# Kernel optimization log

Measured on AMD Instinct MI355X. Metric: run time of the kernel, lower is better.

## Reference

```python
import jax, jax.numpy as jnp
import numpy as np

N, E, D, C, L, G = 50000, 1600000, 128, 10, 4, 512
BN_EPS = 1e-5


def setup_inputs() -> dict:
    key = jax.random.key(0)
    ks = jax.random.split(key, 16)
    s = 0.05  # weight init scale
    inp = {
        "x": jax.random.normal(ks[0], (N, D), dtype=jnp.float32),
        "edge_index": jax.random.randint(ks[1], (2, E), 0, N, dtype=jnp.int32),
        "batch": jnp.sort(jax.random.randint(ks[2], (N,), 0, G, dtype=jnp.int32)),
        "num_graphs": G,
        # GINConv inner MLP params (layer 0 input dim == D since num_features == num_hidden)
        "conv_W1": jax.random.normal(ks[3], (L, D, D), dtype=jnp.float32) * s,
        "conv_b1": jnp.zeros((L, D), dtype=jnp.float32),
        "conv_bn_g": jnp.ones((L, D), dtype=jnp.float32),
        "conv_bn_b": jnp.zeros((L, D), dtype=jnp.float32),
        "conv_W2": jax.random.normal(ks[4], (L, D, D), dtype=jnp.float32) * s,
        "conv_b2": jnp.zeros((L, D), dtype=jnp.float32),
        # outer BatchNorm after each conv
        "bn_g": jnp.ones((L, D), dtype=jnp.float32),
        "bn_b": jnp.zeros((L, D), dtype=jnp.float32),
        # per-scale classifier heads (L+1 of them; fcs[0] input dim == num_features == D)
        "fc_W": jax.random.normal(ks[5], (L + 1, D, C), dtype=jnp.float32) * s,
        "fc_b": jnp.zeros((L + 1, C), dtype=jnp.float32),
    }
    return inp


def _bn(h, g, b):
    # BatchNorm1d in training mode: batch stats over nodes, biased variance
    m = h.mean(axis=0)
    v = jnp.mean((h - m) ** 2, axis=0)
    return (h - m) * jax.lax.rsqrt(v + BN_EPS) * g + b


def reference(x, edge_index, batch, num_graphs, conv_W1, conv_b1, conv_bn_g,
              conv_bn_b, conv_W2, conv_b2, bn_g, bn_b, fc_W, fc_b):
    n_nodes = x.shape[0]
    src, dst = edge_index[0], edge_index[1]
    outs = [x]
    h = x
    for i in range(L):
        # GINConv (eps=0, aggr='add'): mlp(x + scatter_add of neighbor features)
        agg = jax.ops.segment_sum(h[src], dst, num_segments=n_nodes)  # [N, D]
        z = h + agg
        z = z @ conv_W1[i] + conv_b1[i]
        z = jax.nn.relu(_bn(z, conv_bn_g[i], conv_bn_b[i]))
        z = z @ conv_W2[i] + conv_b2[i]
        h = jax.nn.relu(_bn(z, bn_g[i], bn_b[i]))
        outs.append(h)
    out = None
    for i, o in enumerate(outs):
        pooled = jax.ops.segment_sum(o, batch, num_segments=num_graphs)  # [G, D]
        logits = pooled @ fc_W[i] + fc_b[i]
        out = logits if out is None else out + logits
    return jax.nn.log_softmax(out, axis=-1)
```

## Files before the change

kernel.cpp:

```cpp
#include <hip/hip_runtime.h>

#define NN 50000
#define EE 1600000
#define DD 128
#define CC 10
#define LLAY 4
#define GG 512
#define GD (GG*DD)
#define NB 196
#define BK_EDGES 1600
#define BUCKCAP 16000
#define NSUB 16
#define SUBW 3125
#define WPAD 136

static constexpr float BN_EPS = 1e-5f;
static constexpr float INV_N = 1.0f / (float)NN;

typedef __bf16 bf16x8 __attribute__((ext_vector_type(8)));
typedef float f32x4 __attribute__((ext_vector_type(4)));

static __device__ __forceinline__ float bflo(unsigned u){ return __uint_as_float(u << 16); }
static __device__ __forceinline__ float bfhi(unsigned u){ return __uint_as_float(u & 0xffff0000u); }
static __device__ __forceinline__ unsigned short f2bf(float f){
    unsigned u = __float_as_uint(f);
    return (unsigned short)((u + 0x7fffu + ((u >> 16) & 1u)) >> 16);
}
static __device__ __forceinline__ unsigned packbf(float a, float b){
    return (unsigned)f2bf(a) | ((unsigned)f2bf(b) << 16);
}
static __device__ __forceinline__ bf16x8 ldfrag(const unsigned short* p){
    union { uint4 u; bf16x8 b; } t; t.u = *(const uint4*)p; return t.b;
}
static __device__ __forceinline__ bf16x8 asfrag(uint4 u){
    union { uint4 u; bf16x8 b; } t; t.u = u; return t.b;
}


__global__ void zero_k(int* p, int n){
    int i = blockIdx.x * 256 + threadIdx.x;
    if (i < n) p[i] = 0;
}

__global__ void wprep_k(const float* __restrict__ W1, const float* __restrict__ W2,
                        unsigned short* __restrict__ Wtall){
    int idx = blockIdx.x * 256 + threadIdx.x;
    int mat = idx >> 14; int rr = idx & 16383;
    int k = rr >> 7; int j = rr & 127;
    const float* Wsrc = (mat < 4) ? (W1 + mat * 16384) : (W2 + (mat - 4) * 16384);
    Wtall[mat * 16384 + j * 128 + k] = f2bf(Wsrc[k * 128 + j]);
}

__global__ void gsearch_k(const int* __restrict__ batch, int* __restrict__ gstart){
    int g = blockIdx.x * 256 + threadIdx.x;
    if (g <= GG){
        int lo = 0, hi = NN;
        while (lo < hi){ int mid = (lo + hi) >> 1; if (batch[mid] < g) lo = mid + 1; else hi = mid; }
        gstart[g] = lo;
    }
}

__global__ __launch_bounds__(256) void binA_k(const int* __restrict__ srcA,
                                              const int* __restrict__ dstA,
                                              int* __restrict__ bucketCur,
                                              unsigned* __restrict__ binned){
    __shared__ int cnt[NB], bas[NB], off[NB];
    int tid = threadIdx.x;
    if (tid < NB){ cnt[tid] = 0; off[tid] = 0; }
    __syncthreads();
    int e0 = blockIdx.x * BK_EDGES;
    for (int i = tid; i < BK_EDGES; i += 256){
        int e = e0 + i;
        if (e < EE) atomicAdd(&cnt[dstA[e] >> 8], 1);
    }
    __syncthreads();
    if (tid < NB && cnt[tid] > 0) bas[tid] = atomicAdd(&bucketCur[tid], cnt[tid]);
    __syncthreads();
    for (int i = tid; i < BK_EDGES; i += 256){
        int e = e0 + i;
        if (e < EE){
            int d = dstA[e]; int b = d >> 8;
            int p = b * BUCKCAP + bas[b] + atomicAdd(&off[b], 1);
            binned[p] = (unsigned)srcA[e] | ((unsigned)(d & 255) << 17);
        }
    }
}

__global__ __launch_bounds__(256) void bscan_k(const int* __restrict__ bucketCur,
                                               int* __restrict__ bucketBase,
                                               int* __restrict__ rp){
    __shared__ int lds[256];
    int t = threadIdx.x;
    int v = (t < NB) ? bucketCur[t] : 0;
    lds[t] = v; __syncthreads();
    for (int o = 1; o < 256; o <<= 1){
        int xv = 0; if (t >= o) xv = lds[t - o];
        __syncthreads(); lds[t] += xv; __syncthreads();
    }
    int excl = lds[t] - v;
    if (t < NB) bucketBase[t] = excl;
    if (t == 0){ bucketBase[NB] = EE; rp[NN] = EE; }
}

__global__ __launch_bounds__(1024) void binB_k(const unsigned* __restrict__ binned,
                                               const int* __restrict__ bucketCur,
                                               const int* __restrict__ bucketBase,
                                               int* __restrict__ rp,
                                               int* __restrict__ ssort){
    __shared__ int c16[256 * NSUB];
    __shared__ int b16[256 * NSUB];
    __shared__ int nt[256];
    int b = blockIdx.x, tid = threadIdx.x;
    int nb0 = b * 256;
    int nmax = NN - nb0; if (nmax > 256) nmax = 256;
    for (int i = tid; i < 256 * NSUB; i += 1024) c16[i] = 0;
    __syncthreads();
    int cntb = bucketCur[b];
    int src0 = b * BUCKCAP;
    int base = bucketBase[b];
    for (int i = tid; i < cntb; i += 1024){
        unsigned u = binned[src0 + i];
        int src = (int)(u & 0x1FFFFu); int dl = (int)(u >> 17);
        atomicAdd(&c16[dl * NSUB + src / SUBW], 1);
    }
    __syncthreads();
    int cc[NSUB]; int tot = 0;
    if (tid < 256){
        #pragma unroll
        for (int k = 0; k < NSUB; k++){ cc[k] = c16[tid * NSUB + k]; tot += cc[k]; }
        nt[tid] = tot;
    }
    __syncthreads();
    for (int o = 1; o < 256; o <<= 1){
        int xv = 0;
        if (tid < 256 && tid >= o) xv = nt[tid - o];
        __syncthreads();
        if (tid < 256) nt[tid] += xv;
        __syncthreads();
    }
    if (tid < 256){
        int p = base + nt[tid] - tot;
        if (tid < nmax) rp[nb0 + tid] = p;
        int run = p;
        #pragma unroll
        for (int k = 0; k < NSUB; k++){ b16[tid * NSUB + k] = run; run += cc[k]; }
    }
    __syncthreads();
    for (int i = tid; i < 256 * NSUB; i += 1024) c16[i] = 0;
    __syncthreads();
    for (int i = tid; i < cntb; i += 1024){
        unsigned u = binned[src0 + i];
        int src = (int)(u & 0x1FFFFu); int dl = (int)(u >> 17);
        int t = src / SUBW;
        int pos = b16[dl * NSUB + t] + atomicAdd(&c16[dl * NSUB + t], 1);
        ssort[pos] = src;
    }
}

__global__ __launch_bounds__(256) void convxpool_k(const float2* __restrict__ x2,
                                                   const int* __restrict__ gstart,
                                                   unsigned* __restrict__ h32,
                                                   float* __restrict__ outp){
    __shared__ float sd[512];
    int b = blockIdx.x; int gid = b >> 2, chunk = b & 3;
    int tid = threadIdx.x; int c = tid & 63, rs = tid >> 6;
    int s = gstart[gid], e = gstart[gid + 1];
    float a0 = 0.f, a1 = 0.f;
    for (int n = s + chunk * 4 + rs; n < e; n += 16){
        float2 v = x2[n * 64 + c];
        h32[n * 64 + c] = packbf(v.x, v.y);
        a0 += v.x; a1 += v.y;
    }
    sd[tid] = a0; sd[256 + tid] = a1; __syncthreads();
    if (tid < 64){
        float r0 = 0.f, r1 = 0.f;
        #pragma unroll
        for (int k2 = 0; k2 < 4; k2++){ r0 += sd[tid + 64 * k2]; r1 += sd[256 + tid + 64 * k2]; }
        atomicAdd(&outp[gid * 128 + 2 * tid], r0);
        atomicAdd(&outp[gid * 128 + 2 * tid + 1], r1);
    }
}


__global__ __launch_bounds__(256) void agg_k(const unsigned* __restrict__ h32,
                                             const int* __restrict__ rp,
                                             const int* __restrict__ ssort,
                                             unsigned* __restrict__ z32,
                                             float* __restrict__ zstats){
    int tid = threadIdx.x;
    if (blockIdx.x == 0) zstats[tid] = 0.f;
    int n = blockIdx.x * 4 + (tid >> 6);
    int lane = tid & 63;
    unsigned self = h32[n * 64 + lane];
    float ax = bflo(self), ay = bfhi(self);
    int e  = __builtin_amdgcn_readfirstlane(rp[n]);
    int e1 = __builtin_amdgcn_readfirstlane(rp[n + 1]);
    for (; e + 15 < e1; e += 16){
        int sA[16];
        #pragma unroll
        for (int k = 0; k < 16; k++) sA[k] = ssort[e + k];
        unsigned uA[16];
        #pragma unroll
        for (int k = 0; k < 16; k++) uA[k] = h32[sA[k] * 64 + lane];
        #pragma unroll
        for (int k = 0; k < 16; k++){ ax += bflo(uA[k]); ay += bfhi(uA[k]); }
    }
    for (; e + 3 < e1; e += 4){
        int s0 = ssort[e], s1 = ssort[e + 1], s2 = ssort[e + 2], s3 = ssort[e + 3];
        unsigned u0 = h32[s0 * 64 + lane];
        unsigned u1 = h32[s1 * 64 + lane];
        unsigned u2 = h32[s2 * 64 + lane];
        unsigned u3 = h32[s3 * 64 + lane];
        ax += bflo(u0) + bflo(u1); ay += bfhi(u0) + bfhi(u1);
        ax += bflo(u2) + bflo(u3); ay += bfhi(u2) + bfhi(u3);
    }
    for (; e < e1; ++e){
        unsigned u0 = h32[ssort[e] * 64 + lane];
        ax += bflo(u0); ay += bfhi(u0);
    }
    z32[n * 64 + lane] = packbf(ax, ay);
}

template<int TR>
__global__ __launch_bounds__(256) void gemm_k(const unsigned* __restrict__ A32,
                                              const unsigned short* __restrict__ Wtg,
                                              const float* __restrict__ bias,
                                              unsigned short* __restrict__ Cst,
                                              const float* __restrict__ stats,
                                              const float* __restrict__ gma,
                                              const float* __restrict__ bta,
                                              float* __restrict__ ostats,
                                              float* __restrict__ zstats,
                                              float* __restrict__ zpool){
    __shared__ __align__(16) unsigned short Wl[64 * WPAD];
    __shared__ float sred[512];
    __shared__ __align__(16) float sl[128], tl[128];
    int tid = threadIdx.x;
    int slice = blockIdx.x & 1;
    int tileb = blockIdx.x >> 1;

    int wv = tid >> 6, lane = tid & 63;
    int rowbase = tileb * 128 + wv * 32;
    int r0 = rowbase + (lane & 15);
    int r1 = r0 + 16;
    int kd = (lane >> 4) * 4;
    uint4 va[4], vb[4];
    #pragma unroll
    for (int ks = 0; ks < 4; ks++){
        va[ks] = (r0 < NN) ? *(const uint4*)(A32 + r0 * 64 + ks * 16 + kd) : make_uint4(0,0,0,0);
        vb[ks] = (r1 < NN) ? *(const uint4*)(A32 + r1 * 64 + ks * 16 + kd) : make_uint4(0,0,0,0);
    }

    if (blockIdx.x == 0 && zstats) zstats[tid] = 0.f;
    if (zpool && blockIdx.x < 256) zpool[blockIdx.x * 256 + tid] = 0.f;
    {
        const uint4* src = (const uint4*)(Wtg + slice * 64 * 128);
        uint4* dst = (uint4*)Wl;
        #pragma unroll
        for (int i = 0; i < 4; i++){
            int idx = tid + 256 * i;
            int row = idx >> 4, c16 = idx & 15;
            dst[row * (WPAD / 8) + c16] = src[idx];
        }
    }
    if (TR && tid < 128){
        float mean = stats[tid] * INV_N;
        float q    = stats[128 + tid] * INV_N;
        float inv  = rsqrtf(q - mean * mean + BN_EPS);
        float s    = gma[tid] * inv;
        sl[tid] = s; tl[tid] = bta[tid] - mean * s;
    }
    __syncthreads();

    if (TR){
        #pragma unroll
        for (int ks = 0; ks < 4; ks++){
            int q = ks * 8 + (lane >> 4) * 2;
            float4 sA = ((const float4*)sl)[q], sB = ((const float4*)sl)[q + 1];
            float4 tA = ((const float4*)tl)[q], tB = ((const float4*)tl)[q + 1];
            float fs[8] = {sA.x, sA.y, sA.z, sA.w, sB.x, sB.y, sB.z, sB.w};
            float ft[8] = {tA.x, tA.y, tA.z, tA.w, tB.x, tB.y, tB.z, tB.w};
            unsigned* pa = (unsigned*)&va[ks];
            unsigned* pb = (unsigned*)&vb[ks];
            #pragma unroll
            for (int c = 0; c < 4; c++){
                float f0 = fmaxf(bflo(pa[c]) * fs[2*c] + ft[2*c], 0.f);
                float f1 = fmaxf(bfhi(pa[c]) * fs[2*c+1] + ft[2*c+1], 0.f);
                pa[c] = packbf(f0, f1);
                f0 = fmaxf(bflo(pb[c]) * fs[2*c] + ft[2*c], 0.f);
                f1 = fmaxf(bfhi(pb[c]) * fs[2*c+1] + ft[2*c+1], 0.f);
                pb[c] = packbf(f0, f1);
            }
        }
    }

    f32x4 acc[2][4];
    #pragma unroll
    for (int a = 0; a < 2; a++)
        #pragma unroll
        for (int b = 0; b < 4; b++) acc[a][b] = (f32x4){0.f, 0.f, 0.f, 0.f};

    #pragma unroll
    for (int ks = 0; ks < 4; ks++){
        int wk = ks * 32 + (lane >> 4) * 8;
        bf16x8 a0 = asfrag(va[ks]);
        bf16x8 a1 = asfrag(vb[ks]);
        #pragma unroll
        for (int ct = 0; ct < 4; ++ct){
            bf16x8 b = ldfrag(&Wl[(ct * 16 + (lane & 15)) * WPAD + wk]);
            acc[0][ct] = __builtin_amdgcn_mfma_f32_16x16x32_bf16(a0, b, acc[0][ct], 0, 0, 0);
            acc[1][ct] = __builtin_amdgcn_mfma_f32_16x16x32_bf16(a1, b, acc[1][ct], 0, 0, 0);
        }
    }

    int cl = lane & 15, rq = lane >> 4;
    float colS[4], colQ[4];
    #pragma unroll
    for (int ct = 0; ct < 4; ++ct){
        int col = slice * 64 + ct * 16 + cl;
        float bv = bias[col];
        float ps = 0.f, pq = 0.f;
        #pragma unroll
        for (int rt = 0; rt < 2; ++rt){
            #pragma unroll
            for (int rr2 = 0; rr2 < 4; ++rr2){
                int grow = rowbase + rt * 16 + rq * 4 + rr2;
                if (grow < NN){
                    float val = acc[rt][ct][rr2] + bv;
                    Cst[grow * 128 + col] = f2bf(val);
                    ps += val; pq += val * val;
                }
            }
        }
        ps += __shfl_xor(ps, 16); pq += __shfl_xor(pq, 16);
        ps += __shfl_xor(ps, 32); pq += __shfl_xor(pq, 32);
        colS[ct] = ps; colQ[ct] = pq;
    }
    if (rq == 0){
        #pragma unroll
        for (int ct = 0; ct < 4; ++ct){
            sred[wv * 64 + ct * 16 + cl]       = colS[ct];
            sred[256 + wv * 64 + ct * 16 + cl] = colQ[ct];
        }
    }
    __syncthreads();
    if (tid < 64){
        float s1 = sred[tid] + sred[64 + tid] + sred[128 + tid] + sred[192 + tid];
        float s2 = sred[256 + tid] + sred[320 + tid] + sred[384 + tid] + sred[448 + tid];
        atomicAdd(&ostats[slice * 64 + tid], s1);
        atomicAdd(&ostats[128 + slice * 64 + tid], s2);
    }
}

__global__ __launch_bounds__(256) void ewpool_k(const unsigned* __restrict__ z32,
                                                const float* __restrict__ stats,
                                                const float* __restrict__ g,
                                                const float* __restrict__ b,
                                                const int* __restrict__ gstart,
                                                unsigned* __restrict__ h32,
                                                float* __restrict__ outp){
    __shared__ float sd[512];
    int blk = blockIdx.x; int gid = blk >> 2, chunk = blk & 3;
    int tid = threadIdx.x;
    int c = tid & 63, rs = tid >> 6;
    int c2 = c * 2;
    float m0 = stats[c2] * INV_N,     q0 = stats[128 + c2] * INV_N;
    float inv0 = rsqrtf(q0 - m0 * m0 + BN_EPS);
    float s0 = g[c2] * inv0, t0 = b[c2] - m0 * s0;
    float m1 = stats[c2 + 1] * INV_N, q1 = stats[129 + c2] * INV_N;
    float inv1 = rsqrtf(q1 - m1 * m1 + BN_EPS);
    float s1 = g[c2 + 1] * inv1, t1 = b[c2 + 1] - m1 * s1;
    int s = gstart[gid], e = gstart[gid + 1];
    float a0 = 0.f, a1 = 0.f;
    int n = s + chunk * 4 + rs;
    for (; n + 16 < e; n += 32){
        unsigned u0 = z32[n * 64 + c];
        unsigned u1 = z32[(n + 16) * 64 + c];
        float f0, f1;
        f0 = fmaxf(bflo(u0) * s0 + t0, 0.f); f1 = fmaxf(bfhi(u0) * s1 + t1, 0.f);
        h32[n * 64 + c] = packbf(f0, f1); a0 += f0; a1 += f1;
        f0 = fmaxf(bflo(u1) * s0 + t0, 0.f); f1 = fmaxf(bfhi(u1) * s1 + t1, 0.f);
        h32[(n + 16) * 64 + c] = packbf(f0, f1); a0 += f0; a1 += f1;
    }
    for (; n < e; n += 16){
        unsigned u = z32[n * 64 + c];
        float f0 = fmaxf(bflo(u) * s0 + t0, 0.f);
        float f1 = fmaxf(bfhi(u) * s1 + t1, 0.f);
        h32[n * 64 + c] = packbf(f0, f1);
        a0 += f0; a1 += f1;
    }
    sd[tid] = a0; sd[256 + tid] = a1; __syncthreads();
    if (tid < 64){
        float r0 = 0.f, r1 = 0.f;
        #pragma unroll
        for (int k2 = 0; k2 < 4; k2++){ r0 += sd[tid + 64 * k2]; r1 += sd[256 + tid + 64 * k2]; }
        atomicAdd(&outp[gid * 128 + 2 * tid], r0);
        atomicAdd(&outp[gid * 128 + 2 * tid + 1], r1);
    }
}

__global__ __launch_bounds__(64) void final_k(const float* __restrict__ pooled,
                                              const float* __restrict__ fcW,
                                              const float* __restrict__ fcb,
                                              float* __restrict__ out){
    int g = blockIdx.x, l = threadIdx.x;
    float p0[5], p1[5];
    #pragma unroll
    for (int i = 0; i < 5; i++){
        p0[i] = pooled[i * GD + g * 128 + l];
        p1[i] = pooled[i * GD + g * 128 + 64 + l];
    }
    float lg[10];
    #pragma unroll
    for (int c2 = 0; c2 < 10; c2++){
        float s = 0;
        #pragma unroll
        for (int i = 0; i < 5; i++){
            s += p0[i] * fcW[(i * 128 + l) * 10 + c2];
            s += p1[i] * fcW[(i * 128 + 64 + l) * 10 + c2];
        }
        #pragma unroll
        for (int off = 32; off >= 1; off >>= 1) s += __shfl_down(s, off);
        lg[c2] = s;
    }
    if (l == 0){
        #pragma unroll
        for (int c2 = 0; c2 < 10; c2++){
            float bs = 0;
            #pragma unroll
            for (int i = 0; i < 5; i++) bs += fcb[i * 10 + c2];
            lg[c2] += bs;
        }
        float mx = lg[0];
        #pragma unroll
        for (int c2 = 1; c2 < 10; c2++) mx = fmaxf(mx, lg[c2]);
        float se = 0;
        #pragma unroll
        for (int c2 = 0; c2 < 10; c2++) se += expf(lg[c2] - mx);
        float lse = mx + logf(se);
        #pragma unroll
        for (int c2 = 0; c2 < 10; c2++) out[g * 10 + c2] = lg[c2] - lse;
    }
}


extern "C" void kernel_launch(void* const* d_in, const int* in_sizes, int n_in,
                              void* d_out, int out_size, void* d_ws, size_t ws_size,
                              hipStream_t stream){
    (void)in_sizes; (void)n_in; (void)out_size; (void)ws_size;
    const float* x     = (const float*)d_in[0];
    const int*   ei    = (const int*)d_in[1];
    const int*   batch = (const int*)d_in[2];
    const float* cW1   = (const float*)d_in[4];
    const float* cb1   = (const float*)d_in[5];
    const float* cbng  = (const float*)d_in[6];
    const float* cbnb  = (const float*)d_in[7];
    const float* cW2   = (const float*)d_in[8];
    const float* cb2   = (const float*)d_in[9];
    const float* bng   = (const float*)d_in[10];
    const float* bnb   = (const float*)d_in[11];
    const float* fcW   = (const float*)d_in[12];
    const float* fcb   = (const float*)d_in[13];

    char* base = (char*)d_ws;
    size_t off = 0;
    auto alloc = [&](size_t bytes) -> void* {
        void* p = base + off;
        off = (off + bytes + 255) & ~(size_t)255;
        return p;
    };
    unsigned*       hB     = (unsigned*)alloc((size_t)NN * 64 * 4);
    unsigned*       zA     = (unsigned*)alloc((size_t)NN * 64 * 4);
    unsigned*       zB     = (unsigned*)alloc((size_t)NN * 64 * 4);
    unsigned short* Wtall  = (unsigned short*)alloc(8 * 16384 * 2);
    int*            ssort  = (int*)alloc((size_t)EE * 4);
    int*            rp     = (int*)alloc((NN + 1) * 4);
    int*            gstart = (int*)alloc((GG + 1) * 4);
    int*            bucketBase = (int*)alloc((NB + 1) * 4);
    int*            bucketCur  = (int*)alloc(NB * 4);
    float*          pooled = (float*)alloc((size_t)5 * GD * 4);
    float*          stats1 = (float*)alloc(256 * 4);
    float*          stats2 = (float*)alloc(256 * 4);
    unsigned*       binned = (unsigned*)zB;

    int zwords = (int)(((char*)(pooled + GD) - (char*)bucketCur) / 4);

    zero_k<<<(zwords + 255) / 256, 256, 0, stream>>>(bucketCur, zwords);
    wprep_k<<<512, 256, 0, stream>>>(cW1, cW2, Wtall);
    gsearch_k<<<3, 256, 0, stream>>>(batch, gstart);
    binA_k<<<(EE + BK_EDGES - 1) / BK_EDGES, 256, 0, stream>>>(ei, ei + EE, bucketCur, binned);
    bscan_k<<<1, 256, 0, stream>>>(bucketCur, bucketBase, rp);
    binB_k<<<NB, 1024, 0, stream>>>(binned, bucketCur, bucketBase, rp, ssort);
    convxpool_k<<<4 * GG, 256, 0, stream>>>((const float2*)x, gstart, hB, pooled);

    const int gemmGrid = 2 * ((NN + 127) / 128);
    for (int i = 0; i < LLAY; i++){
        agg_k<<<NN / 4, 256, 0, stream>>>(hB, rp, ssort, zA, stats1);
        gemm_k<0><<<gemmGrid, 256, 0, stream>>>(zA, Wtall + i * 16384, cb1 + i * 128,
                                                (unsigned short*)zB,
                                                nullptr, nullptr, nullptr, stats1, stats2, nullptr);
        gemm_k<1><<<gemmGrid, 256, 0, stream>>>(zB, Wtall + (4 + i) * 16384, cb2 + i * 128,
                                                (unsigned short*)zA,
                                                stats1, cbng + i * 128, cbnb + i * 128, stats2, nullptr,
                                                pooled + (size_t)(i + 1) * GD);
        ewpool_k<<<4 * GG, 256, 0, stream>>>(zA, stats2, bng + i * 128, bnb + i * 128,
                                             gstart, hB, pooled + (size_t)(i + 1) * GD);
    }
    final_k<<<GG, 64, 0, stream>>>(pooled, fcW, fcb, (float*)d_out);
}
```

Before: 544.7 us.

## Vectorize neighbor gather with 16-byte loads and add XCD-aware block swizzle

The aggregation kernel now has each 64-lane wavefront split into four groups of 16 lanes. Each lane loads a uint4, so one wavefront gathers four neighbor rows per instruction instead of one. The per-group partial sums are combined with cross-lane shuffles, and one group adds the node's own features and writes the result. Block indices are also remapped so that consecutive nodes land on the same XCD, which should improve L2 locality. The change cuts load instruction count and raises bytes in flight, at the cost of shuffle reductions and idle lanes in the tail and in the final write.

After: 557.4 us. +2.3%, slower.

```diff
diff --git a/kernel.cpp b/kernel.cpp
--- a/kernel.cpp
+++ b/kernel.cpp
@@ -189,36 +189,67 @@
                                              float* __restrict__ zstats){
     int tid = threadIdx.x;
     if (blockIdx.x == 0) zstats[tid] = 0.f;
-    int n = blockIdx.x * 4 + (tid >> 6);
+    const int q = (NN / 4) >> 3, r = (NN / 4) & 7;
+    int xcd = blockIdx.x & 7, ord = blockIdx.x >> 3;
+    int swz = (xcd < r) ? (xcd * (q + 1) + ord)
+                        : (r * (q + 1) + (xcd - r) * q + ord);
+    int n = swz * 4 + (tid >> 6);
     int lane = tid & 63;
-    unsigned self = h32[n * 64 + lane];
-    float ax = bflo(self), ay = bfhi(self);
+    int grp = lane >> 4;
+    int cq  = lane & 15;
+    const uint4* hv = (const uint4*)h32;
     int e  = __builtin_amdgcn_readfirstlane(rp[n]);
     int e1 = __builtin_amdgcn_readfirstlane(rp[n + 1]);
+    float ac[8];
+    #pragma unroll
+    for (int i = 0; i < 8; i++) ac[i] = 0.f;
     for (; e + 15 < e1; e += 16){
-        int sA[16];
-        #pragma unroll
-        for (int k = 0; k < 16; k++) sA[k] = ssort[e + k];
-        unsigned uA[16];
-        #pragma unroll
-        for (int k = 0; k < 16; k++) uA[k] = h32[sA[k] * 64 + lane];
-        #pragma unroll
-        for (int k = 0; k < 16; k++){ ax += bflo(uA[k]); ay += bfhi(uA[k]); }
+        int s[4]; uint4 v[4];
+        #pragma unroll
+        for (int k = 0; k < 4; k++) s[k] = ssort[e + k * 4 + grp];
+        #pragma unroll
+        for (int k = 0; k < 4; k++) v[k] = hv[s[k] * 16 + cq];
+        #pragma unroll
+        for (int k = 0; k < 4; k++){
+            ac[0] += bflo(v[k].x); ac[1] += bfhi(v[k].x);
+            ac[2] += bflo(v[k].y); ac[3] += bfhi(v[k].y);
+            ac[4] += bflo(v[k].z); ac[5] += bfhi(v[k].z);
+            ac[6] += bflo(v[k].w); ac[7] += bfhi(v[k].w);
+        }
     }
     for (; e + 3 < e1; e += 4){
-        int s0 = ssort[e], s1 = ssort[e + 1], s2 = ssort[e + 2], s3 = ssort[e + 3];
-        unsigned u0 = h32[s0 * 64 + lane];
-        unsigned u1 = h32[s1 * 64 + lane];
-        unsigned u2 = h32[s2 * 64 + lane];
-        unsigned u3 = h32[s3 * 64 + lane];
-        ax += bflo(u0) + bflo(u1); ay += bfhi(u0) + bfhi(u1);
-        ax += bflo(u2) + bflo(u3); ay += bfhi(u2) + bfhi(u3);
-    }
-    for (; e < e1; ++e){
-        unsigned u0 = h32[ssort[e] * 64 + lane];
-        ax += bflo(u0); ay += bfhi(u0);
-    }
-    z32[n * 64 + lane] = packbf(ax, ay);
+        int s0 = ssort[e + grp];
+        uint4 v0 = hv[s0 * 16 + cq];
+        ac[0] += bflo(v0.x); ac[1] += bfhi(v0.x);
+        ac[2] += bflo(v0.y); ac[3] += bfhi(v0.y);
+        ac[4] += bflo(v0.z); ac[5] += bfhi(v0.z);
+        ac[6] += bflo(v0.w); ac[7] += bfhi(v0.w);
+    }
+    {
+        int rem = e1 - e;
+        if (grp < rem){
+            int s0 = ssort[e + grp];
+            uint4 v0 = hv[s0 * 16 + cq];
+            ac[0] += bflo(v0.x); ac[1] += bfhi(v0.x);
+            ac[2] += bflo(v0.y); ac[3] += bfhi(v0.y);
+            ac[4] += bflo(v0.z); ac[5] += bfhi(v0.z);
+            ac[6] += bflo(v0.w); ac[7] += bfhi(v0.w);
+        }
+    }
+    #pragma unroll
+    for (int i = 0; i < 8; i++){
+        ac[i] += __shfl_xor(ac[i], 16);
+        ac[i] += __shfl_xor(ac[i], 32);
+    }
+    if (grp == 0){
+        uint4 sv = hv[n * 16 + cq];
+        uint4 o;
+        o.x = packbf(ac[0] + bflo(sv.x), ac[1] + bfhi(sv.x));
+        o.y = packbf(ac[2] + bflo(sv.y), ac[3] + bfhi(sv.y));
+        o.z = packbf(ac[4] + bflo(sv.z), ac[5] + bfhi(sv.z));
+        o.w = packbf(ac[6] + bflo(sv.w), ac[7] + bfhi(sv.w));
+        ((uint4*)z32)[n * 16 + cq] = o;
+    }
 }
 
 template<int TR>
```

## Split neighbor aggregation across XCDs by feature quarter with 16-bit edge indices

Applied to the files above, without the earlier changes.

Aggregation now maps block IDs to XCDs so that each pair of XCDs gathers only one quarter of the feature columns for half the nodes. This keeps each XCD's gather working set small enough to fit in its L2. Each wave processes 16 edges at once with 16-byte vector loads and reduces the partial sums with cross-lane shuffles. The sorted source indices are stored as 16-bit values, which halves index traffic. The cost is four times as many blocks, repeated index reads per feature quarter, and shuffle reduction overhead.

Result: slower. 692.5 us (+27.1%).

```diff
diff --git a/kernel.cpp b/kernel.cpp
--- a/kernel.cpp
+++ b/kernel.cpp
@@ -106,7 +106,7 @@
                                                const int* __restrict__ bucketCur,
                                                const int* __restrict__ bucketBase,
                                                int* __restrict__ rp,
-                                               int* __restrict__ ssort){
+                                               unsigned short* __restrict__ ssort16){
     __shared__ int c16[256 * NSUB];
     __shared__ int b16[256 * NSUB];
     __shared__ int nt[256];
@@ -153,7 +153,7 @@
         int src = (int)(u & 0x1FFFFu); int dl = (int)(u >> 17);
         int t = src / SUBW;
         int pos = b16[dl * NSUB + t] + atomicAdd(&c16[dl * NSUB + t], 1);
-        ssort[pos] = src;
+        ssort16[pos] = (unsigned short)src;
     }
 }
 
@@ -184,41 +184,72 @@
 
 __global__ __launch_bounds__(256) void agg_k(const unsigned* __restrict__ h32,
                                              const int* __restrict__ rp,
-                                             const int* __restrict__ ssort,
+                                             const unsigned short* __restrict__ ssort16,
                                              unsigned* __restrict__ z32,
                                              float* __restrict__ zstats){
     int tid = threadIdx.x;
     if (blockIdx.x == 0) zstats[tid] = 0.f;
-    int n = blockIdx.x * 4 + (tid >> 6);
+    int xcd = blockIdx.x & 7, ord = blockIdx.x >> 3;
+    int g = xcd >> 1, d = xcd & 1;
+    int n = d * (NN / 2) + ord * 4 + (tid >> 6);
     int lane = tid & 63;
-    unsigned self = h32[n * 64 + lane];
-    float ax = bflo(self), ay = bfhi(self);
+    int eslot = lane >> 2;
+    int c = lane & 3;
+    int sbase = g * 4 + c;
+    const uint4* hv = (const uint4*)h32;
     int e  = __builtin_amdgcn_readfirstlane(rp[n]);
     int e1 = __builtin_amdgcn_readfirstlane(rp[n + 1]);
-    for (; e + 15 < e1; e += 16){
-        int sA[16];
-        #pragma unroll
-        for (int k = 0; k < 16; k++) sA[k] = ssort[e + k];
-        unsigned uA[16];
-        #pragma unroll
-        for (int k = 0; k < 16; k++) uA[k] = h32[sA[k] * 64 + lane];
-        #pragma unroll
-        for (int k = 0; k < 16; k++){ ax += bflo(uA[k]); ay += bfhi(uA[k]); }
-    }
-    for (; e + 3 < e1; e += 4){
-        int s0 = ssort[e], s1 = ssort[e + 1], s2 = ssort[e + 2], s3 = ssort[e + 3];
-        unsigned u0 = h32[s0 * 64 + lane];
-        unsigned u1 = h32[s1 * 64 + lane];
-        unsigned u2 = h32[s2 * 64 + lane];
-        unsigned u3 = h32[s3 * 64 + lane];
-        ax += bflo(u0) + bflo(u1); ay += bfhi(u0) + bfhi(u1);
-        ax += bflo(u2) + bflo(u3); ay += bfhi(u2) + bfhi(u3);
-    }
-    for (; e < e1; ++e){
-        unsigned u0 = h32[ssort[e] * 64 + lane];
-        ax += bflo(u0); ay += bfhi(u0);
-    }
-    z32[n * 64 + lane] = packbf(ax, ay);
+    float ac[8];
+    #pragma unroll
+    for (int i = 0; i < 8; i++) ac[i] = 0.f;
+    for (; e + 31 < e1; e += 32){
+        int sA = (int)ssort16[e + eslot];
+        int sB = (int)ssort16[e + 16 + eslot];
+        uint4 vA = hv[sA * 16 + sbase];
+        uint4 vB = hv[sB * 16 + sbase];
+        ac[0] += bflo(vA.x); ac[1] += bfhi(vA.x);
+        ac[2] += bflo(vA.y); ac[3] += bfhi(vA.y);
+        ac[4] += bflo(vA.z); ac[5] += bfhi(vA.z);
+        ac[6] += bflo(vA.w); ac[7] += bfhi(vA.w);
+        ac[0] += bflo(vB.x); ac[1] += bfhi(vB.x);
+        ac[2] += bflo(vB.y); ac[3] += bfhi(vB.y);
+        ac[4] += bflo(vB.z); ac[5] += bfhi(vB.z);
+        ac[6] += bflo(vB.w); ac[7] += bfhi(vB.w);
+    }
+    if (e + 15 < e1){
+        int sA = (int)ssort16[e + eslot];
+        uint4 vA = hv[sA * 16 + sbase];
+        ac[0] += bflo(vA.x); ac[1] += bfhi(vA.x);
+        ac[2] += bflo(vA.y); ac[3] += bfhi(vA.y);
+        ac[4] += bflo(vA.z); ac[5] += bfhi(vA.z);
+        ac[6] += bflo(vA.w); ac[7] += bfhi(vA.w);
+        e += 16;
+    }
+    int rem = e1 - e;
+    if (eslot < rem){
+        int sA = (int)ssort16[e + eslot];
+        uint4 vA = hv[sA * 16 + sbase];
+        ac[0] += bflo(vA.x); ac[1] += bfhi(vA.x);
+        ac[2] += bflo(vA.y); ac[3] += bfhi(vA.y);
+        ac[4] += bflo(vA.z); ac[5] += bfhi(vA.z);
+        ac[6] += bflo(vA.w); ac[7] += bfhi(vA.w);
+    }
+    #pragma unroll
+    for (int i = 0; i < 8; i++){
+        ac[i] += __shfl_xor(ac[i], 4);
+        ac[i] += __shfl_xor(ac[i], 8);
+        ac[i] += __shfl_xor(ac[i], 16);
+        ac[i] += __shfl_xor(ac[i], 32);
+    }
+    if (lane < 4){
+        uint4 sv = hv[n * 16 + sbase];
+        uint4 o;
+        o.x = packbf(ac[0] + bflo(sv.x), ac[1] + bfhi(sv.x));
+        o.y = packbf(ac[2] + bflo(sv.y), ac[3] + bfhi(sv.y));
+        o.z = packbf(ac[4] + bflo(sv.z), ac[5] + bfhi(sv.z));
+        o.w = packbf(ac[6] + bflo(sv.w), ac[7] + bfhi(sv.w));
+        ((uint4*)z32)[n * 16 + sbase] = o;
+    }
 }
 
 template<int TR>
@@ -473,7 +504,7 @@
     unsigned*       zA     = (unsigned*)alloc((size_t)NN * 64 * 4);
     unsigned*       zB     = (unsigned*)alloc((size_t)NN * 64 * 4);
     unsigned short* Wtall  = (unsigned short*)alloc(8 * 16384 * 2);
-    int*            ssort  = (int*)alloc((size_t)EE * 4);
+    unsigned short* ssort16 = (unsigned short*)alloc((size_t)EE * 2);
     int*            rp     = (int*)alloc((NN + 1) * 4);
     int*            gstart = (int*)alloc((GG + 1) * 4);
     int*            bucketBase = (int*)alloc((NB + 1) * 4);
@@ -490,12 +521,12 @@
     gsearch_k<<<3, 256, 0, stream>>>(batch, gstart);
     binA_k<<<(EE + BK_EDGES - 1) / BK_EDGES, 256, 0, stream>>>(ei, ei + EE, bucketCur, binned);
     bscan_k<<<1, 256, 0, stream>>>(bucketCur, bucketBase, rp);
-    binB_k<<<NB, 1024, 0, stream>>>(binned, bucketCur, bucketBase, rp, ssort);
+    binB_k<<<NB, 1024, 0, stream>>>(binned, bucketCur, bucketBase, rp, ssort16);
     convxpool_k<<<4 * GG, 256, 0, stream>>>((const float2*)x, gstart, hB, pooled);
 
     const int gemmGrid = 2 * ((NN + 127) / 128);
     for (int i = 0; i < LLAY; i++){
-        agg_k<<<NN / 4, 256, 0, stream>>>(hB, rp, ssort, zA, stats1);
+        agg_k<<<NN, 256, 0, stream>>>(hB, rp, ssort16, zA, stats1);
         gemm_k<0><<<gemmGrid, 256, 0, stream>>>(zA, Wtall + i * 16384, cb1 + i * 128,
                                                 (unsigned short*)zB,
                                                 nullptr, nullptr, nullptr, stats1, stats2, nullptr);
```

## Fuse neighbor aggregation with first GEMM and pre-zero per-layer stats buffers

Applied to the files above, without the earlier changes.

Merges the gather-sum aggregation kernel and the first MLP GEMM into a single kernel. Each 512-thread block aggregates 128 nodes into shared memory, then runs bf16 MFMA against both weight halves and writes the output plus BN statistics, so the aggregated tensor never makes a round trip through global memory and one launch per layer is removed. The stats buffers become per-layer and are zeroed once up front instead of inside kernels. In exchange, each block's GEMM phase waits on its slowest node's gather, and the larger shared-memory footprint may reduce occupancy.

Measured after the change: 564.6 us. 1.04x slower.

```diff
diff --git a/kernel.cpp b/kernel.cpp
--- a/kernel.cpp
+++ b/kernel.cpp
@@ -13,6 +13,7 @@
 #define NSUB 16
 #define SUBW 3125
 #define WPAD 136
+#define ZPAD 68
 
 static constexpr float BN_EPS = 1e-5f;
 static constexpr float INV_N = 1.0f / (float)NN;
@@ -182,43 +183,140 @@
 }
 
 
-__global__ __launch_bounds__(256) void agg_k(const unsigned* __restrict__ h32,
-                                             const int* __restrict__ rp,
-                                             const int* __restrict__ ssort,
-                                             unsigned* __restrict__ z32,
-                                             float* __restrict__ zstats){
+__global__ __launch_bounds__(512, 6) void aggemm_k(const unsigned* __restrict__ h32,
+                                                   const int* __restrict__ rp,
+                                                   const int* __restrict__ ssort,
+                                                   const unsigned short* __restrict__ Wtg,
+                                                   const float* __restrict__ bias,
+                                                   unsigned short* __restrict__ Cst,
+                                                   float* __restrict__ ostats){
+    __shared__ __align__(16) unsigned zt[128 * ZPAD];
+    __shared__ __align__(16) unsigned short Wl[64 * WPAD];
     int tid = threadIdx.x;
-    if (blockIdx.x == 0) zstats[tid] = 0.f;
-    int n = blockIdx.x * 4 + (tid >> 6);
-    int lane = tid & 63;
-    unsigned self = h32[n * 64 + lane];
-    float ax = bflo(self), ay = bfhi(self);
-    int e  = __builtin_amdgcn_readfirstlane(rp[n]);
-    int e1 = __builtin_amdgcn_readfirstlane(rp[n + 1]);
-    for (; e + 15 < e1; e += 16){
-        int sA[16];
-        #pragma unroll
-        for (int k = 0; k < 16; k++) sA[k] = ssort[e + k];
-        unsigned uA[16];
-        #pragma unroll
-        for (int k = 0; k < 16; k++) uA[k] = h32[sA[k] * 64 + lane];
-        #pragma unroll
-        for (int k = 0; k < 16; k++){ ax += bflo(uA[k]); ay += bfhi(uA[k]); }
-    }
-    for (; e + 3 < e1; e += 4){
-        int s0 = ssort[e], s1 = ssort[e + 1], s2 = ssort[e + 2], s3 = ssort[e + 3];
-        unsigned u0 = h32[s0 * 64 + lane];
-        unsigned u1 = h32[s1 * 64 + lane];
-        unsigned u2 = h32[s2 * 64 + lane];
-        unsigned u3 = h32[s3 * 64 + lane];
-        ax += bflo(u0) + bflo(u1); ay += bfhi(u0) + bfhi(u1);
-        ax += bflo(u2) + bflo(u3); ay += bfhi(u2) + bfhi(u3);
-    }
-    for (; e < e1; ++e){
-        unsigned u0 = h32[ssort[e] * 64 + lane];
-        ax += bflo(u0); ay += bfhi(u0);
-    }
-    z32[n * 64 + lane] = packbf(ax, ay);
+    int w = tid >> 6, lane = tid & 63;
+    int brow = blockIdx.x * 128;
+
+    {
+        const uint4* src = (const uint4*)Wtg;
+        uint4* dst = (uint4*)Wl;
+        #pragma unroll
+        for (int i2 = 0; i2 < 2; i2++){
+            int idx = tid + 512 * i2;
+            int row = idx >> 4, c16 = idx & 15;
+            dst[row * 17 + c16] = src[idx];
+        }
+    }
+
+    for (int i = 0; i < 16; i++){
+        int n = brow + w * 16 + i;
+        float ax = 0.f, ay = 0.f;
+        if (n < NN){
+            unsigned self = h32[n * 64 + lane];
+            ax = bflo(self); ay = bfhi(self);
+            int e  = __builtin_amdgcn_readfirstlane(rp[n]);
+            int e1 = __builtin_amdgcn_readfirstlane(rp[n + 1]);
+            for (; e + 15 < e1; e += 16){
+                int sA[16];
+                #pragma unroll
+                for (int k = 0; k < 16; k++) sA[k] = ssort[e + k];
+                unsigned uA[16];
+                #pragma unroll
+                for (int k = 0; k < 16; k++) uA[k] = h32[sA[k] * 64 + lane];
+                #pragma unroll
+                for (int k = 0; k < 16; k++){ ax += bflo(uA[k]); ay += bfhi(uA[k]); }
+            }
+            for (; e + 3 < e1; e += 4){
+                int s0 = ssort[e], s1 = ssort[e + 1], s2 = ssort[e + 2], s3 = ssort[e + 3];
+                unsigned u0 = h32[s0 * 64 + lane];
+                unsigned u1 = h32[s1 * 64 + lane];
+                unsigned u2 = h32[s2 * 64 + lane];
+                unsigned u3 = h32[s3 * 64 + lane];
+                ax += bflo(u0) + bflo(u1); ay += bfhi(u0) + bfhi(u1);
+                ax += bflo(u2) + bflo(u3); ay += bfhi(u2) + bfhi(u3);
+            }
+            for (; e < e1; ++e){
+                unsigned u0 = h32[ssort[e] * 64 + lane];
+                ax += bflo(u0); ay += bfhi(u0);
+            }
+        }
+        zt[(w * 16 + i) * ZPAD + lane] = packbf(ax, ay);
+    }
+    __syncthreads();
+
+    int rloc = w * 16 + (lane & 15);
+    int kd = (lane >> 4) * 4;
+    bf16x8 af[4];
+    #pragma unroll
+    for (int ks = 0; ks < 4; ks++)
+        af[ks] = asfrag(*(const uint4*)(&zt[rloc * ZPAD + ks * 16 + kd]));
+
+    f32x4 acc[8];
+    #pragma unroll
+    for (int ct = 0; ct < 8; ct++) acc[ct] = (f32x4){0.f, 0.f, 0.f, 0.f};
+
+    #pragma unroll
+    for (int ks = 0; ks < 4; ks++){
+        int wk = ks * 32 + (lane >> 4) * 8;
+        #pragma unroll
+        for (int ct = 0; ct < 4; ++ct){
+            bf16x8 b = ldfrag(&Wl[(ct * 16 + (lane & 15)) * WPAD + wk]);
+            acc[ct] = __builtin_amdgcn_mfma_f32_16x16x32_bf16(af[ks], b, acc[ct], 0, 0, 0);
+        }
+    }
+    __syncthreads();
+    {
+        const uint4* src = (const uint4*)(Wtg + 64 * 128);
+        uint4* dst = (uint4*)Wl;
+        #pragma unroll
+        for (int i2 = 0; i2 < 2; i2++){
+            int idx = tid + 512 * i2;
+            int row = idx >> 4, c16 = idx & 15;
+            dst[row * 17 + c16] = src[idx];
+        }
+    }
+    __syncthreads();
+    #pragma unroll
+    for (int ks = 0; ks < 4; ks++){
+        int wk = ks * 32 + (lane >> 4) * 8;
+        #pragma unroll
+        for (int ct = 0; ct < 4; ++ct){
+            bf16x8 b = ldfrag(&Wl[(ct * 16 + (lane & 15)) * WPAD + wk]);
+            acc[4 + ct] = __builtin_amdgcn_mfma_f32_16x16x32_bf16(af[ks], b, acc[4 + ct], 0, 0, 0);
+        }
+    }
+    __syncthreads();
+
+    float* sred = (float*)Wl;
+    int cl = lane & 15, rq = lane >> 4;
+    #pragma unroll
+    for (int ct = 0; ct < 8; ++ct){
+        int col = ct * 16 + cl;
+        float bv = bias[col];
+        float ps = 0.f, pq = 0.f;
+        #pragma unroll
+        for (int rr2 = 0; rr2 < 4; ++rr2){
+            int grow = brow + w * 16 + rq * 4 + rr2;
+            if (grow < NN){
+                float val = acc[ct][rr2] + bv;
+                Cst[grow * 128 + col] = f2bf(val);
+                ps += val; pq += val * val;
+            }
+        }
+        ps += __shfl_xor(ps, 16); pq += __shfl_xor(pq, 16);
+        ps += __shfl_xor(ps, 32); pq += __shfl_xor(pq, 32);
+        if (rq == 0){
+            sred[w * 128 + col] = ps;
+            sred[1024 + w * 128 + col] = pq;
+        }
+    }
+    __syncthreads();
+    if (tid < 128){
+        float s1 = 0.f, s2 = 0.f;
+        #pragma unroll
+        for (int k = 0; k < 8; k++){ s1 += sred[k * 128 + tid]; s2 += sred[1024 + k * 128 + tid]; }
+        atomicAdd(&ostats[tid], s1);
+        atomicAdd(&ostats[128 + tid], s2);
+    }
 }
 
 template<int TR>
@@ -229,9 +327,7 @@
                                               const float* __restrict__ stats,
                                               const float* __restrict__ gma,
                                               const float* __restrict__ bta,
-                                              float* __restrict__ ostats,
-                                              float* __restrict__ zstats,
-                                              float* __restrict__ zpool){
+                                              float* __restrict__ ostats){
     __shared__ __align__(16) unsigned short Wl[64 * WPAD];
     __shared__ float sred[512];
     __shared__ __align__(16) float sl[128], tl[128];
@@ -251,8 +347,6 @@
         vb[ks] = (r1 < NN) ? *(const uint4*)(A32 + r1 * 64 + ks * 16 + kd) : make_uint4(0,0,0,0);
     }
 
-    if (blockIdx.x == 0 && zstats) zstats[tid] = 0.f;
-    if (zpool && blockIdx.x < 256) zpool[blockIdx.x * 256 + tid] = 0.f;
     {
         const uint4* src = (const uint4*)(Wtg + slice * 64 * 128);
         uint4* dst = (uint4*)Wl;
@@ -479,11 +573,11 @@
     int*            bucketBase = (int*)alloc((NB + 1) * 4);
     int*            bucketCur  = (int*)alloc(NB * 4);
     float*          pooled = (float*)alloc((size_t)5 * GD * 4);
-    float*          stats1 = (float*)alloc(256 * 4);
-    float*          stats2 = (float*)alloc(256 * 4);
+    float*          stats1 = (float*)alloc(LLAY * 256 * 4);
+    float*          stats2 = (float*)alloc(LLAY * 256 * 4);
     unsigned*       binned = (unsigned*)zB;
 
-    int zwords = (int)(((char*)(pooled + GD) - (char*)bucketCur) / 4);
+    int zwords = (int)(((char*)(stats2 + LLAY * 256) - (char*)bucketCur) / 4);
 
     zero_k<<<(zwords + 255) / 256, 256, 0, stream>>>(bucketCur, zwords);
     wprep_k<<<512, 256, 0, stream>>>(cW1, cW2, Wtall);
@@ -493,17 +587,17 @@
     binB_k<<<NB, 1024, 0, stream>>>(binned, bucketCur, bucketBase, rp, ssort);
     convxpool_k<<<4 * GG, 256, 0, stream>>>((const float2*)x, gstart, hB, pooled);
 
-    const int gemmGrid = 2 * ((NN + 127) / 128);
+    const int fusedGrid = (NN + 127) / 128;
+    const int gemmGrid  = 2 * ((NN + 127) / 128);
     for (int i = 0; i < LLAY; i++){
-        agg_k<<<NN / 4, 256, 0, stream>>>(hB, rp, ssort, zA, stats1);
-        gemm_k<0><<<gemmGrid, 256, 0, stream>>>(zA, Wtall + i * 16384, cb1 + i * 128,
-                                                (unsigned short*)zB,
-                                                nullptr, nullptr, nullptr, stats1, stats2, nullptr);
+        aggemm_k<<<fusedGrid, 512, 0, stream>>>(hB, rp, ssort, Wtall + i * 16384,
+                                                cb1 + i * 128, (unsigned short*)zB,
+                                                stats1 + i * 256);
         gemm_k<1><<<gemmGrid, 256, 0, stream>>>(zB, Wtall + (4 + i) * 16384, cb2 + i * 128,
                                                 (unsigned short*)zA,
-                                                stats1, cbng + i * 128, cbnb + i * 128, stats2, nullptr,
-                                                pooled + (size_t)(i + 1) * GD);
-        ewpool_k<<<4 * GG, 256, 0, stream>>>(zA, stats2, bng + i * 128, bnb + i * 128,
+                                                stats1 + i * 256, cbng + i * 128, cbnb + i * 128,
+                                                stats2 + i * 256);
+        ewpool_k<<<4 * GG, 256, 0, stream>>>(zA, stats2 + i * 256, bng + i * 128, bnb + i * 128,
                                              gstart, hB, pooled + (size_t)(i + 1) * GD);
     }
     final_k<<<GG, 64, 0, stream>>>(pooled, fcW, fcb, (float*)d_out);
```
